# Optimization experiments

Measured on AMD Instinct MI355X. Metric: run time of the kernel, lower is better.

The kernel has to match this reference:

```python
import jax, jax.numpy as jnp
import numpy as np

DIM = 96
HEADS = 6
HEAD_DIM = DIM // HEADS  # 16
WIN = 8
N = WIN * WIN            # 64
C = 4 * DIM              # 384
TABLE = (2 * WIN - 1) ** 2  # 225


def setup_inputs() -> dict:
    key = jax.random.key(0)
    ks = jax.random.split(key, 12)
    B_ = 2048  # num_windows * batch = 1024 * 2
    NW = 1024
    x = jax.random.normal(ks[0], (B_, N, C), dtype=jnp.float32)
    cross_x = jax.random.normal(ks[1], (B_, N, C), dtype=jnp.float32)
    rpi = jax.random.randint(ks[2], (N, N), 0, TABLE)
    mask = jnp.zeros((NW, N, N), dtype=jnp.float32)
    s = 0.02
    Wq = jax.random.normal(ks[3], (C, DIM), dtype=jnp.float32) * s
    bq = jnp.zeros((DIM,), dtype=jnp.float32)
    Wk = jax.random.normal(ks[4], (C, DIM), dtype=jnp.float32) * s
    bk = jnp.zeros((DIM,), dtype=jnp.float32)
    Wv = jax.random.normal(ks[5], (C, C), dtype=jnp.float32) * s
    bv = jnp.zeros((C,), dtype=jnp.float32)
    Wp = jax.random.normal(ks[6], (C, C), dtype=jnp.float32) * s
    bp = jnp.zeros((C,), dtype=jnp.float32)
    rpb_table = jax.random.normal(ks[7], (TABLE, HEADS), dtype=jnp.float32) * 0.02
    return {"x": x, "cross_x": cross_x, "rpi": rpi, "mask": mask,
            "Wq": Wq, "bq": bq, "Wk": Wk, "bk": bk, "Wv": Wv, "bv": bv,
            "Wp": Wp, "bp": bp, "rpb_table": rpb_table}


def reference(x, cross_x, rpi, mask, Wq, bq, Wk, bk, Wv, bv, Wp, bp, rpb_table):
    b_, n, c = x.shape
    scale = HEAD_DIM ** (-0.5)
    # projections: q,k -> dim; v -> c (=4*dim)
    q = (x @ Wq + bq).reshape(b_, n, HEADS, HEAD_DIM).transpose(0, 2, 1, 3)
    k = (cross_x @ Wk + bk).reshape(b_, n, HEADS, HEAD_DIM).transpose(0, 2, 1, 3)
    v = (cross_x @ Wv + bv).reshape(b_, n, HEADS, c // HEADS).transpose(0, 2, 1, 3)
    attn = jnp.einsum('bhnd,bhmd->bhnm', q * scale, k)
    # relative position bias: gather (n*n,) indices -> (n, n, heads) -> (heads, n, n)
    bias = rpb_table[rpi.reshape(-1)].reshape(n, n, HEADS).transpose(2, 0, 1)
    attn = attn + bias[None]
    nw = mask.shape[0]
    attn = attn.reshape(b_ // nw, nw, HEADS, n, n) + mask[None, :, None]
    attn = attn.reshape(b_, HEADS, n, n)
    attn = jax.nn.softmax(attn, axis=-1)
    out = jnp.einsum('bhnm,bhmd->bhnd', attn, v)  # (b_, heads, n, c//heads)
    out = out.transpose(0, 2, 1, 3).reshape(b_, n, c)
    out = out @ Wp + bp
    return out
```

## Files before the change

kernel.cpp:

```cpp
#include <hip/hip_runtime.h>
#include <hip/hip_bf16.h>


typedef __attribute__((ext_vector_type(8))) short short8;
typedef __attribute__((ext_vector_type(4))) float f32x4;

__device__ __forceinline__ f32x4 mfma_b16(short8 a, short8 b, f32x4 c) {
  return __builtin_amdgcn_mfma_f32_16x16x32_bf16(a, b, c, 0, 0, 0);
}

__device__ __forceinline__ unsigned short f2bf(float x) {
  return __builtin_bit_cast(unsigned short, __float2bfloat16(x));
}

__device__ __forceinline__ unsigned pack2(float a, float b) {
  return (unsigned)f2bf(a) | ((unsigned)f2bf(b) << 16);
}

__device__ __forceinline__ void gl_lds16(const char* g, char* l) {
  __builtin_amdgcn_global_load_lds(
      (const __attribute__((address_space(1))) unsigned int*)g,
      (__attribute__((address_space(3))) unsigned int*)l, 16, 0, 0);
}

__global__ void prep_k(const float* __restrict__ Wq, const float* __restrict__ Wk,
                       const float* __restrict__ Wv, const float* __restrict__ Wp,
                       const float* __restrict__ rpb, const int* __restrict__ rpi,
                       const float* __restrict__ bk, const float* __restrict__ bv,
                       unsigned short* __restrict__ Wq_t, unsigned short* __restrict__ Wkv_t,
                       unsigned short* __restrict__ Wp_t, float* __restrict__ bias6,
                       float* __restrict__ bias_kv) {
  const int T0 = 96 * 384, T1 = 480 * 384, T2 = 384 * 384, T3 = 6 * 4096, T4 = 480;
  int total = T0 + T1 + T2 + T3 + T4;
  for (int i = blockIdx.x * blockDim.x + threadIdx.x; i < total;
       i += gridDim.x * blockDim.x) {
    int r = i;
    if (r < T0) {
      int n = r / 384, k = r % 384;
      Wq_t[r] = f2bf(Wq[k * 96 + n]);
    } else if ((r -= T0) < T1) {
      int n = r / 384, k = r % 384;
      Wkv_t[r] = f2bf(n < 96 ? Wk[k * 96 + n] : Wv[k * 384 + (n - 96)]);
    } else if ((r -= T1) < T2) {
      int n = r / 384, k = r % 384;
      Wp_t[r] = f2bf(Wp[k * 384 + n]);
    } else if ((r -= T2) < T3) {
      int h = r >> 12, ij = r & 4095;
      bias6[r] = rpb[rpi[ij] * 6 + h];
    } else {
      r -= T3;
      bias_kv[r] = (r < 96) ? bk[r] : bv[r - 96];
    }
  }
}

template <int A_MODE, int OUT_MODE, int NX>
__global__ __launch_bounds__(256, 4) void gemm3_k(
    const void* __restrict__ Av, const unsigned short* __restrict__ Bt,
    const float* __restrict__ bias, void* __restrict__ Outv,
    unsigned short* __restrict__ k_out, unsigned short* __restrict__ vt_out) {
  __shared__ char lds[40960];
  constexpr int AB[2] = {0, 8192}, BB[2] = {16384, 28672};
  const int tid = threadIdx.x, lane = tid & 63, wid = tid >> 6;
  const int g = blockIdx.x;
  const int lg_id = (g & 7) * (NX * 256) + (g >> 3);
  const int my = lg_id / NX, nx = lg_id - my * NX;
  const int m0 = my * 64, n0 = nx * 96;
  const int wm = (wid >> 1) * 32, wn = (wid & 1) * 48;
  const int lr = lane & 15, lg = lane >> 4;

  float4 areg[4];
  const int ar = tid >> 2, aq = tid & 3;

  auto a_issue_f32 = [&](int kt) {
    const float* A = (const float*)Av + (size_t)(m0 + ar) * 384 + kt * 64 + aq * 16;
#pragma unroll
    for (int p = 0; p < 4; ++p) areg[p] = *reinterpret_cast<const float4*>(A + p * 4);
  };
  auto a_write_f32 = [&](char* Ab) {
    unsigned pk[8];
#pragma unroll
    for (int p = 0; p < 4; ++p) {
      pk[p * 2]     = pack2(areg[p].x, areg[p].y);
      pk[p * 2 + 1] = pack2(areg[p].z, areg[p].w);
    }
    const int c0 = aq * 2;
    *reinterpret_cast<uint4*>(Ab + ar * 128 + ((c0 ^ (ar & 7)) * 16)) =
        make_uint4(pk[0], pk[1], pk[2], pk[3]);
    *reinterpret_cast<uint4*>(Ab + ar * 128 + (((c0 + 1) ^ (ar & 7)) * 16)) =
        make_uint4(pk[4], pk[5], pk[6], pk[7]);
  };
  auto b_issue = [&](int kt, char* Bb) {
#pragma unroll
    for (int j = 0; j < 3; ++j) {
      const int rb = (wid * 3 + j) * 8;
      const int row = rb + (lane >> 3), c = lane & 7;
      gl_lds16((const char*)Bt + (size_t)(n0 + row) * 768 + kt * 128 +
                   ((c ^ (row & 7)) * 16),
               Bb + rb * 128);
    }
  };

  f32x4 acc[2][3];
#pragma unroll
  for (int i = 0; i < 2; ++i)
#pragma unroll
    for (int j = 0; j < 3; ++j) acc[i][j] = (f32x4){0.f, 0.f, 0.f, 0.f};

  a_issue_f32(0);
  a_write_f32(lds + AB[0]);
  b_issue(0, lds + BB[0]);
  __syncthreads();

  int cur = 0;
  for (int kt = 0; kt < 6; ++kt) {
    char* An = lds + AB[cur ^ 1];
    char* Bn = lds + BB[cur ^ 1];
    if (kt < 5) {
      a_issue_f32(kt + 1);
      b_issue(kt + 1, Bn);
    }
    {
      const char* Ab = lds + AB[cur];
      const char* Bb = lds + BB[cur];
#pragma unroll
      for (int ks = 0; ks < 2; ++ks) {
        short8 a[2], b[3];
#pragma unroll
        for (int mf = 0; mf < 2; ++mf) {
          const int row = wm + mf * 16 + lr;
          a[mf] = *reinterpret_cast<const short8*>(
              Ab + row * 128 + (((ks * 4 + lg) ^ (row & 7)) * 16));
        }
#pragma unroll
        for (int nf = 0; nf < 3; ++nf) {
          const int row = wn + nf * 16 + lr;
          b[nf] = *reinterpret_cast<const short8*>(
              Bb + row * 128 + (((ks * 4 + lg) ^ (row & 7)) * 16));
        }
#pragma unroll
        for (int mf = 0; mf < 2; ++mf)
#pragma unroll
          for (int nf = 0; nf < 3; ++nf)
            acc[mf][nf] = mfma_b16(a[mf], b[nf], acc[mf][nf]);
      }
    }
    if (kt < 5) a_write_f32(An);
    __syncthreads();
    cur ^= 1;
  }

  if (OUT_MODE == 0 || (OUT_MODE == 2 && nx == 0)) {
    unsigned short* dst = (OUT_MODE == 0) ? (unsigned short*)Outv : k_out;
#pragma unroll
    for (int mf = 0; mf < 2; ++mf)
#pragma unroll
      for (int nf = 0; nf < 3; ++nf) {
        const int col = wn + nf * 16 + lr;
        const float bb = bias[col];
#pragma unroll
        for (int r = 0; r < 4; ++r) {
          const int row = wm + mf * 16 + lg * 4 + r;
          *reinterpret_cast<unsigned short*>(lds + row * 208 + col * 2) =
              f2bf(acc[mf][nf][r] + bb);
        }
      }
    __syncthreads();
#pragma unroll
    for (int j = 0; j < 3; ++j) {
      const int Lb = (j * 256 + tid) * 16;
      const int row = Lb / 192, inner = Lb % 192;
      *reinterpret_cast<uint4*>((char*)dst + (size_t)(m0 + row) * 192 + inner) =
          *reinterpret_cast<const uint4*>(lds + row * 208 + inner);
    }
  } else {
#pragma unroll
    for (int mf = 0; mf < 2; ++mf)
#pragma unroll
      for (int nf = 0; nf < 3; ++nf) {
        const int dl = wn + nf * 16 + lr;
        const float bb = bias[n0 + dl];
        const int tok0 = wm + mf * 16 + lg * 4;
        *reinterpret_cast<unsigned*>(lds + dl * 144 + tok0 * 2) =
            pack2(acc[mf][nf][0] + bb, acc[mf][nf][1] + bb);
        *reinterpret_cast<unsigned*>(lds + dl * 144 + tok0 * 2 + 4) =
            pack2(acc[mf][nf][2] + bb, acc[mf][nf][3] + bb);
      }
    __syncthreads();
#pragma unroll
    for (int j = 0; j < 3; ++j) {
      const int Lc = j * 256 + tid;
      const int dl = Lc >> 3, c = Lc & 7;
      *reinterpret_cast<uint4*>((char*)vt_out + (size_t)my * 49152 +
                                (size_t)((nx - 1) * 96 + dl) * 128 +
                                ((c ^ (dl & 7)) << 4)) =
          *reinterpret_cast<const uint4*>(lds + dl * 144 + c * 16);
    }
  }
}

__global__ __launch_bounds__(256, 2) void ap_k(
    const unsigned short* __restrict__ q_buf, const unsigned short* __restrict__ k_buf,
    const unsigned short* __restrict__ vt_buf, const float* __restrict__ bias6,
    const float* __restrict__ mask, const unsigned short* __restrict__ Wp_t,
    const float* __restrict__ bp, float* __restrict__ out) {
  __shared__ char lds[57344];
  const int tid = threadIdx.x, lane = tid & 63, wid = tid >> 6;
  const int lr = lane & 15, lg = lane >> 4;
  const int w = blockIdx.x;
  char* Pr = lds + 49152;

  const char* vsrc = (const char*)vt_buf + (size_t)w * 49152;
#pragma unroll
  for (int j = 0; j < 12; ++j) {
    const int off = (wid * 12 + j) * 1024;
    gl_lds16(vsrc + off + lane * 16, lds + off);
  }
  __syncthreads();

  unsigned stash[48];
  const float* mw = mask + (size_t)(w & 1023) * 4096;
  const int iq = wid * 16 + lr;

  for (int h = 0; h < 6; ++h) {
    short8 qa = {0, 0, 0, 0, 0, 0, 0, 0};
    if (lg < 2)
      qa = *reinterpret_cast<const short8*>(
          q_buf + (size_t)(w * 64 + iq) * 96 + h * 16 + lg * 8);
    float sv[4][4];
#pragma unroll
    for (int tj = 0; tj < 4; ++tj) {
      short8 kf = {0, 0, 0, 0, 0, 0, 0, 0};
      if (lg < 2)
        kf = *reinterpret_cast<const short8*>(
            k_buf + (size_t)(w * 64 + tj * 16 + lr) * 96 + h * 16 + lg * 8);
      f32x4 z = {0.f, 0.f, 0.f, 0.f};
      f32x4 s = mfma_b16(kf, qa, z);
      const int j0 = tj * 16 + lg * 4;
      const float4 bi = *reinterpret_cast<const float4*>(bias6 + h * 4096 + iq * 64 + j0);
      const float4 mk = *reinterpret_cast<const float4*>(mw + iq * 64 + j0);
      sv[tj][0] = s[0] * 0.25f + bi.x + mk.x;
      sv[tj][1] = s[1] * 0.25f + bi.y + mk.y;
      sv[tj][2] = s[2] * 0.25f + bi.z + mk.z;
      sv[tj][3] = s[3] * 0.25f + bi.w + mk.w;
    }
    float mx = sv[0][0];
#pragma unroll
    for (int tj = 0; tj < 4; ++tj)
#pragma unroll
      for (int r = 0; r < 4; ++r) mx = fmaxf(mx, sv[tj][r]);
    mx = fmaxf(mx, __shfl_xor(mx, 16));
    mx = fmaxf(mx, __shfl_xor(mx, 32));
    float sum = 0.f;
#pragma unroll
    for (int tj = 0; tj < 4; ++tj)
#pragma unroll
      for (int r = 0; r < 4; ++r) {
        sv[tj][r] = __expf(sv[tj][r] - mx);
        sum += sv[tj][r];
      }
    sum += __shfl_xor(sum, 16);
    sum += __shfl_xor(sum, 32);
    const float inv = 1.0f / sum;
#pragma unroll
    for (int tj = 0; tj < 4; ++tj) {
      const int c = tj * 2 + (lg >> 1);
      uint2 st;
      st.x = pack2(sv[tj][0] * inv, sv[tj][1] * inv);
      st.y = pack2(sv[tj][2] * inv, sv[tj][3] * inv);
      *reinterpret_cast<uint2*>(Pr + iq * 128 + ((c ^ (iq & 7)) << 4) +
                                (lg & 1) * 8) = st;
    }
    short8 pa[2];
#pragma unroll
    for (int ks = 0; ks < 2; ++ks)
      pa[ks] = *reinterpret_cast<const short8*>(
          Pr + iq * 128 + (((ks * 4 + lg) ^ (iq & 7)) << 4));
    __builtin_amdgcn_s_setprio(1);
#pragma unroll
    for (int td = 0; td < 4; ++td) {
      f32x4 o = {0.f, 0.f, 0.f, 0.f};
#pragma unroll
      for (int ks = 0; ks < 2; ++ks) {
        const int d = h * 64 + td * 16 + lr;
        short8 vb = *reinterpret_cast<const short8*>(
            lds + d * 128 + (((ks * 4 + lg) ^ (d & 7)) << 4));
        o = mfma_b16(vb, pa[ks], o);
      }
      stash[h * 8 + td * 2 + 0] = pack2(o[0], o[1]);
      stash[h * 8 + td * 2 + 1] = pack2(o[2], o[3]);
    }
    __builtin_amdgcn_s_setprio(0);
  }
  __syncthreads();

  f32x4 acc[4][6];
#pragma unroll
  for (int i = 0; i < 4; ++i)
#pragma unroll
    for (int j = 0; j < 6; ++j) acc[i][j] = (f32x4){0.f, 0.f, 0.f, 0.f};

#pragma unroll 1
  for (int kt = 0; kt < 6; ++kt) {
#pragma unroll
    for (int t = 0; t < 4; ++t)
#pragma unroll
      for (int j = 0; j < 3; ++j) {
        const int rb = (wid * 3 + j) * 8;
        const int row = rb + (lane >> 3), c = lane & 7;
        gl_lds16((const char*)Wp_t + (size_t)(t * 96 + row) * 768 + kt * 128 +
                     ((c ^ (row & 7)) * 16),
                 lds + t * 12288 + rb * 128);
      }
#pragma unroll
    for (int td = 0; td < 4; ++td) {
      uint2 st = make_uint2(stash[kt * 8 + td * 2], stash[kt * 8 + td * 2 + 1]);
      *reinterpret_cast<uint2*>(
          Pr + iq * 128 + (((td * 2 + (lg >> 1)) ^ (iq & 7)) << 4) +
          (lg & 1) * 8) = st;
    }
    short8 a0 = *reinterpret_cast<const short8*>(
        Pr + iq * 128 + (((0 * 4 + lg) ^ (iq & 7)) << 4));
    short8 a1 = *reinterpret_cast<const short8*>(
        Pr + iq * 128 + (((1 * 4 + lg) ^ (iq & 7)) << 4));
    __syncthreads();
    __builtin_amdgcn_s_setprio(1);
#pragma unroll
    for (int t = 0; t < 4; ++t)
#pragma unroll
      for (int ks = 0; ks < 2; ++ks) {
        const short8 a = ks ? a1 : a0;
#pragma unroll
        for (int nf = 0; nf < 6; ++nf) {
          const int row = nf * 16 + lr;
          const short8 b = *reinterpret_cast<const short8*>(
              lds + t * 12288 + row * 128 + (((ks * 4 + lg) ^ (row & 7)) * 16));
          acc[t][nf] = mfma_b16(a, b, acc[t][nf]);
        }
      }
    __builtin_amdgcn_s_setprio(0);
    __syncthreads();
  }

#pragma unroll
  for (int t = 0; t < 4; ++t)
#pragma unroll
    for (int nf = 0; nf < 6; ++nf) {
      const int col = t * 96 + nf * 16 + lr;
      const float bb = bp[col];
#pragma unroll
      for (int r = 0; r < 4; ++r)
        out[(size_t)(w * 64 + wid * 16 + lg * 4 + r) * 384 + col] =
            acc[t][nf][r] + bb;
    }
}

extern "C" void kernel_launch(void* const* d_in, const int* in_sizes, int n_in,
                              void* d_out, int out_size, void* d_ws, size_t ws_size,
                              hipStream_t stream) {
  const float* x    = (const float*)d_in[0];
  const float* cx   = (const float*)d_in[1];
  const int*   rpi  = (const int*)d_in[2];
  const float* mask = (const float*)d_in[3];
  const float* Wq   = (const float*)d_in[4];
  const float* bq   = (const float*)d_in[5];
  const float* Wk   = (const float*)d_in[6];
  const float* bk   = (const float*)d_in[7];
  const float* Wv   = (const float*)d_in[8];
  const float* bv   = (const float*)d_in[9];
  const float* Wp   = (const float*)d_in[10];
  const float* bp   = (const float*)d_in[11];
  const float* rpb  = (const float*)d_in[12];

  char* ws = (char*)d_ws;
  unsigned short* Wq_t   = (unsigned short*)(ws + 0);
  unsigned short* Wkv_t  = (unsigned short*)(ws + 73728);
  unsigned short* Wp_t   = (unsigned short*)(ws + 442368);
  float*          bias6  = (float*)(ws + 737280);
  float*          biaskv = (float*)(ws + 835584);
  const size_t MB = 1u << 20;
  unsigned short* q_buf  = (unsigned short*)(ws + MB);
  unsigned short* k_buf  = (unsigned short*)(ws + MB + 25165824u);
  unsigned short* vt_buf = (unsigned short*)(ws + MB + 50331648u);

  prep_k<<<256, 256, 0, stream>>>(Wq, Wk, Wv, Wp, rpb, rpi, bk, bv,
                                  Wq_t, Wkv_t, Wp_t, bias6, biaskv);
  gemm3_k<0, 0, 1><<<2048, 256, 0, stream>>>(x, Wq_t, bq, q_buf, nullptr, nullptr);
  gemm3_k<0, 2, 5><<<10240, 256, 0, stream>>>(cx, Wkv_t, biaskv, nullptr, k_buf, vt_buf);
  ap_k<<<2048, 256, 0, stream>>>(q_buf, k_buf, vt_buf, bias6, mask, Wp_t, bp,
                                 (float*)d_out);
}
```

Baseline: 378.5 us.

## Process two windows per block to share Wp tiles in output projection

```diff
diff --git a/kernel.cpp b/kernel.cpp
--- a/kernel.cpp
+++ b/kernel.cpp
@@ -15,6 +15,10 @@
 
 __device__ __forceinline__ unsigned pack2(float a, float b) {
   return (unsigned)f2bf(a) | ((unsigned)f2bf(b) << 16);
+}
+
+__device__ __forceinline__ int swz48(int c, int r) {
+  return (c & ~7) | ((c ^ r) & 7);
 }
 
 __device__ __forceinline__ void gl_lds16(const char* g, char* l) {
@@ -207,152 +211,180 @@
   __shared__ char lds[57344];
   const int tid = threadIdx.x, lane = tid & 63, wid = tid >> 6;
   const int lr = lane & 15, lg = lane >> 4;
-  const int w = blockIdx.x;
-  char* Pr = lds + 49152;
-
-  const char* vsrc = (const char*)vt_buf + (size_t)w * 49152;
-#pragma unroll
-  for (int j = 0; j < 12; ++j) {
-    const int off = (wid * 12 + j) * 1024;
-    gl_lds16(vsrc + off + lane * 16, lds + off);
-  }
-  __syncthreads();
-
-  unsigned stash[48];
-  const float* mw = mask + (size_t)(w & 1023) * 4096;
+  const int w0 = blockIdx.x * 2;
   const int iq = wid * 16 + lr;
-
-  for (int h = 0; h < 6; ++h) {
-    short8 qa = {0, 0, 0, 0, 0, 0, 0, 0};
-    if (lg < 2)
-      qa = *reinterpret_cast<const short8*>(
-          q_buf + (size_t)(w * 64 + iq) * 96 + h * 16 + lg * 8);
-    float sv[4][4];
-#pragma unroll
-    for (int tj = 0; tj < 4; ++tj) {
-      short8 kf = {0, 0, 0, 0, 0, 0, 0, 0};
+  char* P0 = lds + 49152;
+  char* P1 = lds + 24576;
+
+  auto stage_vt = [&](int w) {
+    const char* vsrc = (const char*)vt_buf + (size_t)w * 49152;
+#pragma unroll
+    for (int j = 0; j < 12; ++j) {
+      const int off = (wid * 12 + j) * 1024;
+      gl_lds16(vsrc + off + lane * 16, lds + off);
+    }
+  };
+  auto b_issue = [&](int nc, int kt, char* Bb) {
+#pragma unroll
+    for (int j = 0; j < 3; ++j) {
+      const int rb = (wid * 3 + j) * 8;
+      const int row = rb + (lane >> 3), c = lane & 7;
+      gl_lds16((const char*)Wp_t + (size_t)(nc * 96 + row) * 768 + kt * 128 +
+                   ((c ^ (row & 7)) * 16),
+               Bb + rb * 128);
+    }
+  };
+
+  unsigned stash0[48], stash1[48];
+  const float* mw0 = mask + (size_t)(w0 & 1023) * 4096;
+  const float* mw1 = mask + (size_t)((w0 + 1) & 1023) * 4096;
+
+  auto attn_phase = [&](int w, const float* mw, unsigned (&st)[48]) {
+#pragma unroll
+    for (int h = 0; h < 6; ++h) {
+      short8 qa = {0, 0, 0, 0, 0, 0, 0, 0};
       if (lg < 2)
-        kf = *reinterpret_cast<const short8*>(
-            k_buf + (size_t)(w * 64 + tj * 16 + lr) * 96 + h * 16 + lg * 8);
-      f32x4 z = {0.f, 0.f, 0.f, 0.f};
-      f32x4 s = mfma_b16(kf, qa, z);
-      const int j0 = tj * 16 + lg * 4;
-      const float4 bi = *reinterpret_cast<const float4*>(bias6 + h * 4096 + iq * 64 + j0);
-      const float4 mk = *reinterpret_cast<const float4*>(mw + iq * 64 + j0);
-      sv[tj][0] = s[0] * 0.25f + bi.x + mk.x;
-      sv[tj][1] = s[1] * 0.25f + bi.y + mk.y;
-      sv[tj][2] = s[2] * 0.25f + bi.z + mk.z;
-      sv[tj][3] = s[3] * 0.25f + bi.w + mk.w;
-    }
-    float mx = sv[0][0];
-#pragma unroll
-    for (int tj = 0; tj < 4; ++tj)
-#pragma unroll
-      for (int r = 0; r < 4; ++r) mx = fmaxf(mx, sv[tj][r]);
-    mx = fmaxf(mx, __shfl_xor(mx, 16));
-    mx = fmaxf(mx, __shfl_xor(mx, 32));
-    float sum = 0.f;
-#pragma unroll
-    for (int tj = 0; tj < 4; ++tj)
-#pragma unroll
-      for (int r = 0; r < 4; ++r) {
-        sv[tj][r] = __expf(sv[tj][r] - mx);
-        sum += sv[tj][r];
-      }
-    sum += __shfl_xor(sum, 16);
-    sum += __shfl_xor(sum, 32);
-    const float inv = 1.0f / sum;
-#pragma unroll
-    for (int tj = 0; tj < 4; ++tj) {
-      const int c = tj * 2 + (lg >> 1);
-      uint2 st;
-      st.x = pack2(sv[tj][0] * inv, sv[tj][1] * inv);
-      st.y = pack2(sv[tj][2] * inv, sv[tj][3] * inv);
-      *reinterpret_cast<uint2*>(Pr + iq * 128 + ((c ^ (iq & 7)) << 4) +
-                                (lg & 1) * 8) = st;
-    }
-    short8 pa[2];
-#pragma unroll
-    for (int ks = 0; ks < 2; ++ks)
-      pa[ks] = *reinterpret_cast<const short8*>(
-          Pr + iq * 128 + (((ks * 4 + lg) ^ (iq & 7)) << 4));
-    __builtin_amdgcn_s_setprio(1);
-#pragma unroll
-    for (int td = 0; td < 4; ++td) {
-      f32x4 o = {0.f, 0.f, 0.f, 0.f};
+        qa = *reinterpret_cast<const short8*>(
+            q_buf + (size_t)(w * 64 + iq) * 96 + h * 16 + lg * 8);
+      float sv[4][4];
+#pragma unroll
+      for (int tj = 0; tj < 4; ++tj) {
+        short8 kf = {0, 0, 0, 0, 0, 0, 0, 0};
+        if (lg < 2)
+          kf = *reinterpret_cast<const short8*>(
+              k_buf + (size_t)(w * 64 + tj * 16 + lr) * 96 + h * 16 + lg * 8);
+        f32x4 z = {0.f, 0.f, 0.f, 0.f};
+        f32x4 s = mfma_b16(kf, qa, z);
+        const int j0 = tj * 16 + lg * 4;
+        const float4 bi =
+            *reinterpret_cast<const float4*>(bias6 + h * 4096 + iq * 64 + j0);
+        const float4 mk = *reinterpret_cast<const float4*>(mw + iq * 64 + j0);
+        sv[tj][0] = s[0] * 0.25f + bi.x + mk.x;
+        sv[tj][1] = s[1] * 0.25f + bi.y + mk.y;
+        sv[tj][2] = s[2] * 0.25f + bi.z + mk.z;
+        sv[tj][3] = s[3] * 0.25f + bi.w + mk.w;
+      }
+      float mx = sv[0][0];
+#pragma unroll
+      for (int tj = 0; tj < 4; ++tj)
+#pragma unroll
+        for (int r = 0; r < 4; ++r) mx = fmaxf(mx, sv[tj][r]);
+      mx = fmaxf(mx, __shfl_xor(mx, 16));
+      mx = fmaxf(mx, __shfl_xor(mx, 32));
+      float sum = 0.f;
+#pragma unroll
+      for (int tj = 0; tj < 4; ++tj)
+#pragma unroll
+        for (int r = 0; r < 4; ++r) {
+          sv[tj][r] = __expf(sv[tj][r] - mx);
+          sum += sv[tj][r];
+        }
+      sum += __shfl_xor(sum, 16);
+      sum += __shfl_xor(sum, 32);
+      const float inv = 1.0f / sum;
+#pragma unroll
+      for (int tj = 0; tj < 4; ++tj) {
+        const int c = tj * 2 + (lg >> 1);
+        uint2 st2;
+        st2.x = pack2(sv[tj][0] * inv, sv[tj][1] * inv);
+        st2.y = pack2(sv[tj][2] * inv, sv[tj][3] * inv);
+        *reinterpret_cast<uint2*>(P0 + iq * 128 + ((c ^ (iq & 7)) << 4) +
+                                  (lg & 1) * 8) = st2;
+      }
+      short8 pa[2];
+#pragma unroll
+      for (int ks = 0; ks < 2; ++ks)
+        pa[ks] = *reinterpret_cast<const short8*>(
+            P0 + iq * 128 + (((ks * 4 + lg) ^ (iq & 7)) << 4));
+#pragma unroll
+      for (int td = 0; td < 4; ++td) {
+        f32x4 o = {0.f, 0.f, 0.f, 0.f};
+#pragma unroll
+        for (int ks = 0; ks < 2; ++ks) {
+          const int d = h * 64 + td * 16 + lr;
+          short8 vb = *reinterpret_cast<const short8*>(
+              lds + d * 128 + (((ks * 4 + lg) ^ (d & 7)) << 4));
+          o = mfma_b16(vb, pa[ks], o);
+        }
+        st[h * 8 + td * 2 + 0] = pack2(o[0], o[1]);
+        st[h * 8 + td * 2 + 1] = pack2(o[2], o[3]);
+      }
+    }
+  };
+
+  stage_vt(w0);
+  __syncthreads();
+  attn_phase(w0, mw0, stash0);
+  __syncthreads();
+  stage_vt(w0 + 1);
+  __syncthreads();
+  attn_phase(w0 + 1, mw1, stash1);
+  __syncthreads();
+
+  b_issue(0, 0, lds);
+  __syncthreads();
+
+#pragma unroll 1
+  for (int nc = 0; nc < 4; ++nc) {
+    f32x4 acc0[6], acc1[6];
+#pragma unroll
+    for (int j = 0; j < 6; ++j) {
+      acc0[j] = (f32x4){0.f, 0.f, 0.f, 0.f};
+      acc1[j] = (f32x4){0.f, 0.f, 0.f, 0.f};
+    }
+#pragma unroll
+    for (int kt = 0; kt < 6; ++kt) {
+      if (kt < 5) b_issue(nc, kt + 1, lds + ((kt + 1) & 1) * 12288);
+      else if (nc < 3) b_issue(nc + 1, 0, lds);
+      const char* Bb = lds + (kt & 1) * 12288;
+#pragma unroll
+      for (int td = 0; td < 4; ++td) {
+        uint2 s0 = make_uint2(stash0[kt * 8 + td * 2], stash0[kt * 8 + td * 2 + 1]);
+        uint2 s1 = make_uint2(stash1[kt * 8 + td * 2], stash1[kt * 8 + td * 2 + 1]);
+        const int off = iq * 128 + (((td * 2 + (lg >> 1)) ^ (iq & 7)) << 4) +
+                        (lg & 1) * 8;
+        *reinterpret_cast<uint2*>(P0 + off) = s0;
+        *reinterpret_cast<uint2*>(P1 + off) = s1;
+      }
+      short8 a00 = *reinterpret_cast<const short8*>(
+          P0 + iq * 128 + (((0 + lg) ^ (iq & 7)) << 4));
+      short8 a01 = *reinterpret_cast<const short8*>(
+          P0 + iq * 128 + (((4 + lg) ^ (iq & 7)) << 4));
+      short8 a10 = *reinterpret_cast<const short8*>(
+          P1 + iq * 128 + (((0 + lg) ^ (iq & 7)) << 4));
+      short8 a11 = *reinterpret_cast<const short8*>(
+          P1 + iq * 128 + (((4 + lg) ^ (iq & 7)) << 4));
+      __builtin_amdgcn_s_setprio(1);
 #pragma unroll
       for (int ks = 0; ks < 2; ++ks) {
-        const int d = h * 64 + td * 16 + lr;
-        short8 vb = *reinterpret_cast<const short8*>(
-            lds + d * 128 + (((ks * 4 + lg) ^ (d & 7)) << 4));
-        o = mfma_b16(vb, pa[ks], o);
-      }
-      stash[h * 8 + td * 2 + 0] = pack2(o[0], o[1]);
-      stash[h * 8 + td * 2 + 1] = pack2(o[2], o[3]);
-    }
-    __builtin_amdgcn_s_setprio(0);
-  }
-  __syncthreads();
-
-  f32x4 acc[4][6];
-#pragma unroll
-  for (int i = 0; i < 4; ++i)
-#pragma unroll
-    for (int j = 0; j < 6; ++j) acc[i][j] = (f32x4){0.f, 0.f, 0.f, 0.f};
-
-#pragma unroll 1
-  for (int kt = 0; kt < 6; ++kt) {
-#pragma unroll
-    for (int t = 0; t < 4; ++t)
-#pragma unroll
-      for (int j = 0; j < 3; ++j) {
-        const int rb = (wid * 3 + j) * 8;
-        const int row = rb + (lane >> 3), c = lane & 7;
-        gl_lds16((const char*)Wp_t + (size_t)(t * 96 + row) * 768 + kt * 128 +
-                     ((c ^ (row & 7)) * 16),
-                 lds + t * 12288 + rb * 128);
-      }
-#pragma unroll
-    for (int td = 0; td < 4; ++td) {
-      uint2 st = make_uint2(stash[kt * 8 + td * 2], stash[kt * 8 + td * 2 + 1]);
-      *reinterpret_cast<uint2*>(
-          Pr + iq * 128 + (((td * 2 + (lg >> 1)) ^ (iq & 7)) << 4) +
-          (lg & 1) * 8) = st;
-    }
-    short8 a0 = *reinterpret_cast<const short8*>(
-        Pr + iq * 128 + (((0 * 4 + lg) ^ (iq & 7)) << 4));
-    short8 a1 = *reinterpret_cast<const short8*>(
-        Pr + iq * 128 + (((1 * 4 + lg) ^ (iq & 7)) << 4));
-    __syncthreads();
-    __builtin_amdgcn_s_setprio(1);
-#pragma unroll
-    for (int t = 0; t < 4; ++t)
-#pragma unroll
-      for (int ks = 0; ks < 2; ++ks) {
-        const short8 a = ks ? a1 : a0;
+        const short8 a0 = ks ? a01 : a00;
+        const short8 a1 = ks ? a11 : a10;
 #pragma unroll
         for (int nf = 0; nf < 6; ++nf) {
           const int row = nf * 16 + lr;
           const short8 b = *reinterpret_cast<const short8*>(
-              lds + t * 12288 + row * 128 + (((ks * 4 + lg) ^ (row & 7)) * 16));
-          acc[t][nf] = mfma_b16(a, b, acc[t][nf]);
-        }
-      }
-    __builtin_amdgcn_s_setprio(0);
-    __syncthreads();
+              Bb + row * 128 + (((ks * 4 + lg) ^ (row & 7)) * 16));
+          acc0[nf] = mfma_b16(a0, b, acc0[nf]);
+          acc1[nf] = mfma_b16(a1, b, acc1[nf]);
+        }
+      }
+      __builtin_amdgcn_s_setprio(0);
+      if (kt == 5) {
+#pragma unroll
+        for (int nf = 0; nf < 6; ++nf) {
+          const int col = nc * 96 + nf * 16 + lr;
+          const float bb = bp[col];
+#pragma unroll
+          for (int r = 0; r < 4; ++r) {
+            const int rowl = wid * 16 + lg * 4 + r;
+            out[(size_t)(w0 * 64 + rowl) * 384 + col] = acc0[nf][r] + bb;
+            out[(size_t)((w0 + 1) * 64 + rowl) * 384 + col] = acc1[nf][r] + bb;
+          }
+        }
+      }
+      __syncthreads();
+    }
   }
-
-#pragma unroll
-  for (int t = 0; t < 4; ++t)
-#pragma unroll
-    for (int nf = 0; nf < 6; ++nf) {
-      const int col = t * 96 + nf * 16 + lr;
-      const float bb = bp[col];
-#pragma unroll
-      for (int r = 0; r < 4; ++r)
-        out[(size_t)(w * 64 + wid * 16 + lg * 4 + r) * 384 + col] =
-            acc[t][nf][r] + bb;
-    }
 }
 
 extern "C" void kernel_launch(void* const* d_in, const int* in_sizes, int n_in,
@@ -387,6 +419,6 @@
                                   Wq_t, Wkv_t, Wp_t, bias6, biaskv);
   gemm3_k<0, 0, 1><<<2048, 256, 0, stream>>>(x, Wq_t, bq, q_buf, nullptr, nullptr);
   gemm3_k<0, 2, 5><<<10240, 256, 0, stream>>>(cx, Wkv_t, biaskv, nullptr, k_buf, vt_buf);
-  ap_k<<<2048, 256, 0, stream>>>(q_buf, k_buf, vt_buf, bias6, mask, Wp_t, bp,
+  ap_k<<<1024, 256, 0, stream>>>(q_buf, k_buf, vt_buf, bias6, mask, Wp_t, bp,
                                  (float*)d_out);
 }
```

Measured after the change: 355.4 us. 6.1% less time.
